# Kernel tuning notes

Hardware: AMD Instinct MI355X
Metric: run time of the kernel (lower is better)

Reference implementation:

```python
import jax, jax.numpy as jnp
import numpy as np

N = 50000        # nodes
E = 1600000      # edges (before self loops)
C_IN = 128
C_OUT = 128
G = 64           # graphs in the batch
NEG_SLOPE = 0.2  # GATConv default


def setup_inputs() -> dict:
    key = jax.random.key(0)
    ks = jax.random.split(key, 12)
    u = jax.random.normal(ks[0], (N, C_IN), jnp.float32)
    edge_index = jax.random.randint(ks[1], (2, E), 0, N, dtype=jnp.int32)
    batch = jnp.sort(jax.random.randint(ks[2], (N,), 0, G, dtype=jnp.int32))
    g1 = 1.0 / np.sqrt(C_IN)
    g2 = 1.0 / np.sqrt(C_OUT)
    return {
        "u": u,
        "W1": jax.random.normal(ks[3], (C_IN, C_OUT), jnp.float32) * g1,
        "a_src1": jax.random.normal(ks[4], (C_OUT,), jnp.float32) * g2,
        "a_dst1": jax.random.normal(ks[5], (C_OUT,), jnp.float32) * g2,
        "b1": jnp.zeros((C_OUT,), jnp.float32),
        "W2": jax.random.normal(ks[6], (C_OUT, C_OUT), jnp.float32) * g2,
        "a_src2": jax.random.normal(ks[7], (C_OUT,), jnp.float32) * g2,
        "a_dst2": jax.random.normal(ks[8], (C_OUT,), jnp.float32) * g2,
        "b2": jnp.zeros((C_OUT,), jnp.float32),
        "edge_index": edge_index,
        "batch": batch,
    }


def gat_conv(x, edge_index, W, a_src, a_dst, b):
    """PyG GATConv, heads=1: linear -> edge attention -> scatter softmax -> scatter add."""
    n = x.shape[0]
    h = x @ W                                        # [N, C]
    loops = jnp.arange(n, dtype=edge_index.dtype)    # add_self_loops=True
    src = jnp.concatenate([edge_index[0], loops])    # message source j
    dst = jnp.concatenate([edge_index[1], loops])    # aggregation target i
    alpha_s = h @ a_src                              # [N]
    alpha_d = h @ a_dst                              # [N]
    e = jax.nn.leaky_relu(alpha_s[src] + alpha_d[dst], NEG_SLOPE)  # [E+N]
    m = jax.ops.segment_max(e, dst, num_segments=n)  # stable softmax per target
    w = jnp.exp(e - m[dst])
    denom = jax.ops.segment_sum(w, dst, num_segments=n)
    alpha = w / denom[dst]                           # [E+N]
    out = jax.ops.segment_sum(alpha[:, None] * h[src], dst, num_segments=n)
    return out + b


def reference(u, W1, a_src1, a_dst1, b1, W2, a_src2, a_dst2, b2, edge_index, batch):
    h = jax.nn.selu(gat_conv(u, edge_index, W1, a_src1, a_dst1, b1))
    h = jax.nn.selu(gat_conv(h, edge_index, W2, a_src2, a_dst2, b2))
    # global_mean_pool
    s = jax.ops.segment_sum(h, batch, num_segments=G)                      # [G, C]
    cnt = jax.ops.segment_sum(jnp.ones((h.shape[0],), h.dtype), batch, num_segments=G)
    return s / jnp.maximum(cnt, 1.0)[:, None]
```

## Files before the change

kernel.cpp:

```cpp
#include <hip/hip_runtime.h>
#include <hip/hip_bf16.h>
#include <math.h>

#define CH 128
#define PSHIFT 8
#define PSIZE (1 << PSHIFT)
#define CHUNK 2048
#define EPT 8
#define MAXP 256
#define PCAP 12288
#define PS 8

typedef __attribute__((ext_vector_type(8))) short short8;
typedef __attribute__((ext_vector_type(4))) float f32x4;

__device__ __forceinline__ float seluf(float x) {
    const float scale = 1.0507009873554804934193349852946f;
    const float alpha = 1.6732632423543772848170429916717f;
    return x > 0.0f ? scale * x : scale * alpha * (__expf(x) - 1.0f);
}

__device__ __forceinline__ float lrelu(float x) {
    return x > 0.0f ? x : 0.2f * x;
}

__device__ __forceinline__ short bfc(float f) {
    union { __hip_bfloat16 b; short s; } u;
    u.b = __float2bfloat16(f);
    return u.s;
}

__device__ __forceinline__ unsigned pk(float lo, float hi) {
    return ((unsigned)(unsigned short)bfc(hi) << 16) | (unsigned short)bfc(lo);
}


__global__ __launch_bounds__(256) void k_part(const int* __restrict__ ei,
                                              int* __restrict__ pfill,
                                              unsigned long long* __restrict__ staged,
                                              int E, int NP) {
    __shared__ int hist[MAXP];
    __shared__ int base[MAXP];
    const int tid = threadIdx.x;
    const int j0 = blockIdx.x * CHUNK;
    for (int i = tid; i < NP; i += 256) hist[i] = 0;
    __syncthreads();
    int part[EPT], rank[EPT];
    unsigned long long rec[EPT];
#pragma unroll
    for (int e = 0; e < EPT; ++e) {
        int j = j0 + e * 256 + tid;
        part[e] = -1;
        if (j < E) {
            int s = ei[j], d = ei[E + j];
            part[e] = d >> PSHIFT;
            rec[e] = ((unsigned long long)(unsigned)d << 32) | (unsigned)s;
            rank[e] = atomicAdd(&hist[part[e]], 1);
        }
    }
    __syncthreads();
    for (int i = tid; i < NP; i += 256)
        base[i] = hist[i] ? atomicAdd(&pfill[i], hist[i]) : 0;
    __syncthreads();
#pragma unroll
    for (int e = 0; e < EPT; ++e)
        if (part[e] >= 0)
            staged[(size_t)part[e] * PCAP + base[part[e]] + rank[e]] = rec[e];
}


__global__ __launch_bounds__(256) void k_fat(
    const unsigned long long* __restrict__ staged, const int* __restrict__ pfill,
    int* __restrict__ rowptr, int* __restrict__ csr, int n, int E, int NP,
    const float* __restrict__ x, const float* __restrict__ W,
    const float* __restrict__ a_s, const float* __restrict__ a_d,
    __hip_bfloat16* __restrict__ hb, float* __restrict__ as_o,
    float* __restrict__ ad_o) {
    __shared__ __align__(16) char sm[32768];
    const int tid = threadIdx.x;

    if ((int)blockIdx.x < NP) {
        int* lcnt = (int*)sm;
        int* lrow = lcnt + PSIZE;
        int* sc   = lrow + PSIZE;
        int* psc  = sc + PSIZE;
        const int p = blockIdx.x;
        const int d0 = p << PSHIFT;
        psc[tid] = (tid < NP) ? pfill[tid] : 0;
        lcnt[tid] = 0;
        __syncthreads();
        for (int off = 1; off < 256; off <<= 1) {
            int v = (tid >= off) ? psc[tid - off] : 0;
            __syncthreads();
            psc[tid] += v;
            __syncthreads();
        }
        const int pbase = psc[p] - pfill[p];
        const size_t rbeg = (size_t)p * PCAP;
        const size_t rend = rbeg + pfill[p];
        const int rb = pbase + d0;
        for (size_t r = rbeg + tid; r < rend; r += 256)
            atomicAdd(&lcnt[(int)(staged[r] >> 32) - d0], 1);
        __syncthreads();
        int myv = (d0 + tid < n) ? lcnt[tid] + 1 : 0;
        sc[tid] = myv;
        __syncthreads();
        for (int off = 1; off < 256; off <<= 1) {
            int v = (tid >= off) ? sc[tid - off] : 0;
            __syncthreads();
            sc[tid] += v;
            __syncthreads();
        }
        if (d0 + tid < n) {
            int rp = rb + sc[tid] - myv;
            lrow[tid] = rp;
            rowptr[d0 + tid] = rp;
            csr[rp] = d0 + tid;
            lcnt[tid] = 0;
        }
        if (p == 0 && tid == 0) rowptr[n] = E + n;
        __syncthreads();
        for (size_t r = rbeg + tid; r < rend; r += 256) {
            unsigned long long v = staged[r];
            int d = (int)(v >> 32), s = (int)(v & 0xffffffffu);
            int pos = lrow[d - d0] + 1 + atomicAdd(&lcnt[d - d0], 1);
            csr[pos] = s;
        }
        return;
    }

    short* WB = (short*)sm;
    for (int i = tid; i < CH * CH; i += 256) {
        int k = i >> 7, c = i & 127;
        int kb = k >> 5, kk = k & 31;
        int t = c >> 4;
        int ln = (c & 15) | ((kk >> 3) << 4);
        int j = kk & 7;
        WB[(((kb << 3) + t) << 9) + (ln << 3) + j] = bfc(W[i]);
    }
    __syncthreads();
    const int bid = blockIdx.x - NP;
    const int lane = tid & 63;
    const int wid = tid >> 6;
    const int l15 = lane & 15;
    const int lhi = lane >> 4;
    float asl[8], adl[8];
#pragma unroll
    for (int t = 0; t < 8; ++t) {
        asl[t] = a_s[t * 16 + l15];
        adl[t] = a_d[t * 16 + l15];
    }
#pragma unroll
    for (int s = 0; s < 2; ++s) {
        int r0 = bid * 128 + s * 64 + wid * 16;
        if (r0 >= n) break;
        int ar = r0 + l15; if (ar >= n) ar = n - 1;
        const float* xr = x + (size_t)ar * CH + lhi * 8;
        f32x4 acc[8];
#pragma unroll
        for (int t = 0; t < 8; ++t) acc[t] = (f32x4){0.f, 0.f, 0.f, 0.f};
#pragma unroll
        for (int kb = 0; kb < 4; ++kb) {
            float4 xa = *(const float4*)(xr + kb * 32);
            float4 xb = *(const float4*)(xr + kb * 32 + 4);
            short8 af;
            af[0] = bfc(xa.x); af[1] = bfc(xa.y); af[2] = bfc(xa.z); af[3] = bfc(xa.w);
            af[4] = bfc(xb.x); af[5] = bfc(xb.y); af[6] = bfc(xb.z); af[7] = bfc(xb.w);
#pragma unroll
            for (int t = 0; t < 8; ++t) {
                short8 bv = ((const short8*)WB)[(((kb << 3) + t) << 6) | lane];
                acc[t] = __builtin_amdgcn_mfma_f32_16x16x32_bf16(af, bv, acc[t], 0, 0, 0);
            }
        }
        float pa[4] = {0.f, 0.f, 0.f, 0.f}, pd[4] = {0.f, 0.f, 0.f, 0.f};
#pragma unroll
        for (int t = 0; t < 8; ++t) {
#pragma unroll
            for (int q = 0; q < 4; ++q) {
                int row = r0 + lhi * 4 + q;
                if (row < n)
                    hb[(size_t)row * CH + t * 16 + l15] = __float2bfloat16(acc[t][q]);
                pa[q] += acc[t][q] * asl[t];
                pd[q] += acc[t][q] * adl[t];
            }
        }
#pragma unroll
        for (int q = 0; q < 4; ++q) {
#pragma unroll
            for (int o = 1; o < 16; o <<= 1) {
                pa[q] += __shfl_xor(pa[q], o);
                pd[q] += __shfl_xor(pd[q], o);
            }
        }
        if (l15 == 0) {
#pragma unroll
            for (int q = 0; q < 4; ++q) {
                int row = r0 + lhi * 4 + q;
                if (row < n) { as_o[row] = pa[q]; ad_o[row] = pd[q]; }
            }
        }
    }
}


template <typename T>
__global__ __launch_bounds__(256) void k_gemm3(
    const T* __restrict__ x, const float* __restrict__ W,
    const float* __restrict__ a_s, const float* __restrict__ a_d,
    __hip_bfloat16* __restrict__ hb, float* __restrict__ as_o,
    float* __restrict__ ad_o, int n) {
    __shared__ short WB[4 * 8 * 64 * 8];
    const int tid = threadIdx.x;
    for (int i = tid; i < CH * CH; i += 256) {
        int k = i >> 7, c = i & 127;
        int kb = k >> 5, kk = k & 31;
        int t = c >> 4;
        int ln = (c & 15) | ((kk >> 3) << 4);
        int j = kk & 7;
        WB[(((kb << 3) + t) << 9) + (ln << 3) + j] = bfc(W[i]);
    }
    __syncthreads();
    const int lane = tid & 63;
    const int wid = tid >> 6;
    const int l15 = lane & 15;
    const int lhi = lane >> 4;
    float asl[8], adl[8];
#pragma unroll
    for (int t = 0; t < 8; ++t) {
        asl[t] = a_s[t * 16 + l15];
        adl[t] = a_d[t * 16 + l15];
    }
#pragma unroll
    for (int s = 0; s < 2; ++s) {
        int r0 = blockIdx.x * 128 + s * 64 + wid * 16;
        if (r0 >= n) break;
        int ar = r0 + l15; if (ar >= n) ar = n - 1;
        const T* xr = x + (size_t)ar * CH + lhi * 8;
        f32x4 acc[8];
#pragma unroll
        for (int t = 0; t < 8; ++t) acc[t] = (f32x4){0.f, 0.f, 0.f, 0.f};
#pragma unroll
        for (int kb = 0; kb < 4; ++kb) {
            short8 af;
            if constexpr (sizeof(T) == 4) {
                float4 xa = *(const float4*)(xr + kb * 32);
                float4 xb = *(const float4*)(xr + kb * 32 + 4);
                af[0] = bfc(xa.x); af[1] = bfc(xa.y); af[2] = bfc(xa.z); af[3] = bfc(xa.w);
                af[4] = bfc(xb.x); af[5] = bfc(xb.y); af[6] = bfc(xb.z); af[7] = bfc(xb.w);
            } else {
                af = *(const short8*)(xr + kb * 32);
            }
#pragma unroll
            for (int t = 0; t < 8; ++t) {
                short8 bv = ((const short8*)WB)[(((kb << 3) + t) << 6) | lane];
                acc[t] = __builtin_amdgcn_mfma_f32_16x16x32_bf16(af, bv, acc[t], 0, 0, 0);
            }
        }
        float pa[4] = {0.f, 0.f, 0.f, 0.f}, pd[4] = {0.f, 0.f, 0.f, 0.f};
#pragma unroll
        for (int t = 0; t < 8; ++t) {
#pragma unroll
            for (int q = 0; q < 4; ++q) {
                int row = r0 + lhi * 4 + q;
                if (row < n)
                    hb[(size_t)row * CH + t * 16 + l15] = __float2bfloat16(acc[t][q]);
                pa[q] += acc[t][q] * asl[t];
                pd[q] += acc[t][q] * adl[t];
            }
        }
#pragma unroll
        for (int q = 0; q < 4; ++q) {
#pragma unroll
            for (int o = 1; o < 16; o <<= 1) {
                pa[q] += __shfl_xor(pa[q], o);
                pd[q] += __shfl_xor(pd[q], o);
            }
        }
        if (l15 == 0) {
#pragma unroll
            for (int q = 0; q < 4; ++q) {
                int row = r0 + lhi * 4 + q;
                if (row < n) { as_o[row] = pa[q]; ad_o[row] = pd[q]; }
            }
        }
    }
}


__global__ __launch_bounds__(256) void k_fused_agg(
    const int* __restrict__ rowptr, const int* __restrict__ csr,
    const float* __restrict__ as_v, const float* __restrict__ ad_v,
    float* __restrict__ wedge, const __hip_bfloat16* __restrict__ hb,
    const float* __restrict__ bias, __hip_bfloat16* __restrict__ out, int n) {
    int gw = (int)((blockIdx.x * (size_t)blockDim.x + threadIdx.x) >> 6);
    int lane = threadIdx.x & 63;
    if (gw >= n) return;
    int beg = rowptr[gw], end = rowptr[gw + 1];
    int deg = end - beg;
    float adi = ad_v[gw];

    const int quarter = lane >> 4;
    const int c8 = lane & 15;
    float acc[8];
#pragma unroll
    for (int k = 0; k < 8; ++k) acc[k] = 0.f;
    float inv;

    if (deg <= 64) {
        bool valid = lane < deg;
        int src = valid ? csr[beg + lane] : 0;
        float e = valid ? lrelu(as_v[src] + adi) : -1e30f;
        float m = e;
#pragma unroll
        for (int o = 32; o > 0; o >>= 1) m = fmaxf(m, __shfl_xor(m, o));
        float w = valid ? __expf(e - m) : 0.f;
        float s = w;
#pragma unroll
        for (int o = 32; o > 0; o >>= 1) s += __shfl_xor(s, o);
        inv = 1.0f / s;
        for (int b = 0; b < deg; b += 8) {
            int i0 = b + quarter;
            int i1 = b + 4 + quarter;
            float w0 = __shfl(w, i0);
            int s0 = __shfl(src, i0);
            float w1 = (i1 < 64) ? __shfl(w, i1) : 0.f;
            int s1 = (i1 < 64) ? __shfl(src, i1) : 0;
            uint4 hv0 = ((const uint4*)hb)[(size_t)s0 * 16 + c8];
            uint4 hv1 = ((const uint4*)hb)[(size_t)s1 * 16 + c8];
            acc[0] += w0 * __uint_as_float(hv0.x << 16);
            acc[1] += w0 * __uint_as_float(hv0.x & 0xffff0000u);
            acc[2] += w0 * __uint_as_float(hv0.y << 16);
            acc[3] += w0 * __uint_as_float(hv0.y & 0xffff0000u);
            acc[4] += w0 * __uint_as_float(hv0.z << 16);
            acc[5] += w0 * __uint_as_float(hv0.z & 0xffff0000u);
            acc[6] += w0 * __uint_as_float(hv0.w << 16);
            acc[7] += w0 * __uint_as_float(hv0.w & 0xffff0000u);
            acc[0] += w1 * __uint_as_float(hv1.x << 16);
            acc[1] += w1 * __uint_as_float(hv1.x & 0xffff0000u);
            acc[2] += w1 * __uint_as_float(hv1.y << 16);
            acc[3] += w1 * __uint_as_float(hv1.y & 0xffff0000u);
            acc[4] += w1 * __uint_as_float(hv1.z << 16);
            acc[5] += w1 * __uint_as_float(hv1.z & 0xffff0000u);
            acc[6] += w1 * __uint_as_float(hv1.w << 16);
            acc[7] += w1 * __uint_as_float(hv1.w & 0xffff0000u);
        }
    } else {
        float m = -1e30f;
        for (int p = beg + lane; p < end; p += 64) {
            float e = lrelu(as_v[csr[p]] + adi);
            wedge[p] = e;
            m = fmaxf(m, e);
        }
#pragma unroll
        for (int o = 32; o > 0; o >>= 1) m = fmaxf(m, __shfl_xor(m, o));
        float s = 0.f;
        for (int p = beg + lane; p < end; p += 64) {
            float wv = __expf(wedge[p] - m);
            wedge[p] = wv;
            s += wv;
        }
#pragma unroll
        for (int o = 32; o > 0; o >>= 1) s += __shfl_xor(s, o);
        inv = 1.0f / s;
        for (int p = beg; p < end; p += 8) {
            int p0 = p + quarter, p1 = p + 4 + quarter;
            float w0 = 0.f, w1 = 0.f;
            int s0 = 0, s1 = 0;
            if (p0 < end) { w0 = wedge[p0]; s0 = csr[p0]; }
            if (p1 < end) { w1 = wedge[p1]; s1 = csr[p1]; }
            uint4 hv0 = ((const uint4*)hb)[(size_t)s0 * 16 + c8];
            uint4 hv1 = ((const uint4*)hb)[(size_t)s1 * 16 + c8];
            acc[0] += w0 * __uint_as_float(hv0.x << 16);
            acc[1] += w0 * __uint_as_float(hv0.x & 0xffff0000u);
            acc[2] += w0 * __uint_as_float(hv0.y << 16);
            acc[3] += w0 * __uint_as_float(hv0.y & 0xffff0000u);
            acc[4] += w0 * __uint_as_float(hv0.z << 16);
            acc[5] += w0 * __uint_as_float(hv0.z & 0xffff0000u);
            acc[6] += w0 * __uint_as_float(hv0.w << 16);
            acc[7] += w0 * __uint_as_float(hv0.w & 0xffff0000u);
            acc[0] += w1 * __uint_as_float(hv1.x << 16);
            acc[1] += w1 * __uint_as_float(hv1.x & 0xffff0000u);
            acc[2] += w1 * __uint_as_float(hv1.y << 16);
            acc[3] += w1 * __uint_as_float(hv1.y & 0xffff0000u);
            acc[4] += w1 * __uint_as_float(hv1.z << 16);
            acc[5] += w1 * __uint_as_float(hv1.z & 0xffff0000u);
            acc[6] += w1 * __uint_as_float(hv1.w << 16);
            acc[7] += w1 * __uint_as_float(hv1.w & 0xffff0000u);
        }
    }
#pragma unroll
    for (int k = 0; k < 8; ++k) {
        acc[k] += __shfl_xor(acc[k], 16);
        acc[k] += __shfl_xor(acc[k], 32);
    }
    if (quarter == 0) {
        const float4 bv0 = ((const float4*)bias)[c8 * 2];
        const float4 bv1 = ((const float4*)bias)[c8 * 2 + 1];
        float o0 = seluf(acc[0] * inv + bv0.x);
        float o1 = seluf(acc[1] * inv + bv0.y);
        float o2 = seluf(acc[2] * inv + bv0.z);
        float o3 = seluf(acc[3] * inv + bv0.w);
        float o4 = seluf(acc[4] * inv + bv1.x);
        float o5 = seluf(acc[5] * inv + bv1.y);
        float o6 = seluf(acc[6] * inv + bv1.z);
        float o7 = seluf(acc[7] * inv + bv1.w);
        uint4 ov;
        ov.x = pk(o0, o1);
        ov.y = pk(o2, o3);
        ov.z = pk(o4, o5);
        ov.w = pk(o6, o7);
        ((uint4*)out)[(size_t)gw * 16 + c8] = ov;
    }
}


__device__ int lower_bound_dev(const int* a, int n, int key) {
    int lo = 0, hi = n;
    while (lo < hi) {
        int mid = (lo + hi) >> 1;
        if (a[mid] < key) lo = mid + 1; else hi = mid;
    }
    return lo;
}

__global__ __launch_bounds__(256) void k_pool1(const __hip_bfloat16* __restrict__ x,
                                               const int* __restrict__ batchv,
                                               float* __restrict__ part, int n) {
    int g = blockIdx.x >> 3, s = blockIdx.x & (PS - 1);
    int lo = lower_bound_dev(batchv, n, g);
    int hi = lower_bound_dev(batchv, n, g + 1);
    int lane = threadIdx.x & 63, wv = threadIdx.x >> 6;
    int slot = s * 4 + wv;
    float sx0 = 0.f, sy0 = 0.f, sx1 = 0.f, sy1 = 0.f;
    int i = lo + slot;
    for (; i + 32 < hi; i += 64) {
        unsigned u0 = ((const unsigned*)x)[(size_t)i * 64 + lane];
        unsigned u1 = ((const unsigned*)x)[(size_t)(i + 32) * 64 + lane];
        sx0 += __uint_as_float(u0 << 16);
        sy0 += __uint_as_float(u0 & 0xffff0000u);
        sx1 += __uint_as_float(u1 << 16);
        sy1 += __uint_as_float(u1 & 0xffff0000u);
    }
    if (i < hi) {
        unsigned u0 = ((const unsigned*)x)[(size_t)i * 64 + lane];
        sx0 += __uint_as_float(u0 << 16);
        sy0 += __uint_as_float(u0 & 0xffff0000u);
    }
    __shared__ float2 red[4][64];
    red[wv][lane] = make_float2(sx0 + sx1, sy0 + sy1);
    __syncthreads();
    if (wv == 0) {
        float2 a = red[0][lane], b = red[1][lane], c = red[2][lane], d = red[3][lane];
        float* pp = part + ((size_t)(g * PS + s)) * CH;
        pp[2 * lane] = a.x + b.x + c.x + d.x;
        pp[2 * lane + 1] = a.y + b.y + c.y + d.y;
    }
}

__global__ __launch_bounds__(128) void k_pool2(const float* __restrict__ part,
                                               const int* __restrict__ batchv,
                                               float* __restrict__ outp, int n) {
    int g = blockIdx.x, t = threadIdx.x;
    int lo = lower_bound_dev(batchv, n, g);
    int hi = lower_bound_dev(batchv, n, g + 1);
    float v = 0.f;
#pragma unroll
    for (int s = 0; s < PS; ++s) v += part[((size_t)(g * PS + s)) * CH + t];
    int cnt = hi - lo; if (cnt < 1) cnt = 1;
    outp[(size_t)g * CH + t] = v / (float)cnt;
}


extern "C" void kernel_launch(void* const* d_in, const int* in_sizes, int n_in,
                              void* d_out, int out_size, void* d_ws, size_t ws_size,
                              hipStream_t stream) {
    const float* u   = (const float*)d_in[0];
    const float* W1  = (const float*)d_in[1];
    const float* as1 = (const float*)d_in[2];
    const float* ad1 = (const float*)d_in[3];
    const float* b1  = (const float*)d_in[4];
    const float* W2  = (const float*)d_in[5];
    const float* as2 = (const float*)d_in[6];
    const float* ad2 = (const float*)d_in[7];
    const float* b2  = (const float*)d_in[8];
    const int* ei    = (const int*)d_in[9];
    const int* batchv= (const int*)d_in[10];

    const int N = in_sizes[0] / CH;
    const int E = in_sizes[9] / 2;
    const int M = E + N;
    const int NP = (N + PSIZE - 1) >> PSHIFT;
    const int G = out_size / CH;

    char* p = (char*)d_ws;
    auto alloc = [&](size_t bytes) {
        char* r = p;
        p += (bytes + 255) & ~(size_t)255;
        return r;
    };
    int*   pfill  = (int*)alloc((size_t)NP * 4);
    size_t zbytes = (size_t)(p - (char*)d_ws);
    int*   rowptr = (int*)alloc((size_t)(N + 1) * 4);
    int*   csr    = (int*)alloc((size_t)M * 4);
    float* asv    = (float*)alloc((size_t)N * 4);
    float* adv    = (float*)alloc((size_t)N * 4);
    float* ppart  = (float*)alloc((size_t)G * PS * CH * 4);
    __hip_bfloat16* hbuf = (__hip_bfloat16*)alloc((size_t)N * CH * 2);
    size_t wbytes = ((size_t)M * 4 + 255) & ~(size_t)255;
    size_t xbytes = (size_t)N * CH * 2;
    size_t sbytes = (size_t)NP * PCAP * 8;
    size_t blob   = wbytes + xbytes > sbytes ? wbytes + xbytes : sbytes;
    char*  bb     = alloc(blob);
    unsigned long long* staged = (unsigned long long*)bb;
    float* wedge  = (float*)bb;
    __hip_bfloat16* x2 = (__hip_bfloat16*)(bb + wbytes);

    hipMemsetAsync(d_ws, 0, zbytes, stream);

    const int gblocks = (N + 127) / 128;

    k_part<<<(E + CHUNK - 1) / CHUNK, 256, 0, stream>>>(ei, pfill, staged, E, NP);
    k_fat<<<NP + gblocks, 256, 0, stream>>>(staged, pfill, rowptr, csr, N, E, NP,
                                            u, W1, as1, ad1, hbuf, asv, adv);

    k_fused_agg<<<(N * 64 + 255) / 256, 256, 0, stream>>>(rowptr, csr, asv, adv, wedge, hbuf, b1, x2, N);

    k_gemm3<__hip_bfloat16><<<gblocks, 256, 0, stream>>>(x2, W2, as2, ad2, hbuf, asv, adv, N);
    k_fused_agg<<<(N * 64 + 255) / 256, 256, 0, stream>>>(rowptr, csr, asv, adv, wedge, hbuf, b2, x2, N);

    k_pool1<<<G * PS, 256, 0, stream>>>(x2, batchv, ppart, N);
    k_pool2<<<G, 128, 0, stream>>>(ppart, batchv, (float*)d_out, N);
}
```

Baseline: 201.2 us.

## Pack staged edges to 32 bits, unroll gather by four, fuse pooling kernels

Staged edge records now pack the local destination into 8 bits and the source into 24 bits, halving staging traffic. The partition chunk per block doubles. The low-degree aggregation loop now gathers four neighbour rows per iteration to expose more memory parallelism. The two-stage mean pool becomes one 1024-thread kernel per graph, which removes a launch but lowers parallelism and assumes N fits in 24 bits.

New measurement: 190.6 us. 5.3% less time.

```diff
diff --git a/kernel.cpp b/kernel.cpp
--- a/kernel.cpp
+++ b/kernel.cpp
@@ -5,8 +5,8 @@
 #define CH 128
 #define PSHIFT 8
 #define PSIZE (1 << PSHIFT)
-#define CHUNK 2048
-#define EPT 8
+#define CHUNK 4096
+#define EPT 16
 #define MAXP 256
 #define PCAP 12288
 #define PS 8
@@ -37,7 +37,7 @@
 
 __global__ __launch_bounds__(256) void k_part(const int* __restrict__ ei,
                                               int* __restrict__ pfill,
-                                              unsigned long long* __restrict__ staged,
+                                              unsigned* __restrict__ staged,
                                               int E, int NP) {
     __shared__ int hist[MAXP];
     __shared__ int base[MAXP];
@@ -46,7 +46,7 @@
     for (int i = tid; i < NP; i += 256) hist[i] = 0;
     __syncthreads();
     int part[EPT], rank[EPT];
-    unsigned long long rec[EPT];
+    unsigned rec[EPT];
 #pragma unroll
     for (int e = 0; e < EPT; ++e) {
         int j = j0 + e * 256 + tid;
@@ -54,7 +54,7 @@
         if (j < E) {
             int s = ei[j], d = ei[E + j];
             part[e] = d >> PSHIFT;
-            rec[e] = ((unsigned long long)(unsigned)d << 32) | (unsigned)s;
+            rec[e] = ((unsigned)(d & (PSIZE - 1)) << 24) | (unsigned)s;
             rank[e] = atomicAdd(&hist[part[e]], 1);
         }
     }
@@ -70,7 +70,7 @@
 
 
 __global__ __launch_bounds__(256) void k_fat(
-    const unsigned long long* __restrict__ staged, const int* __restrict__ pfill,
+    const unsigned* __restrict__ staged, const int* __restrict__ pfill,
     int* __restrict__ rowptr, int* __restrict__ csr, int n, int E, int NP,
     const float* __restrict__ x, const float* __restrict__ W,
     const float* __restrict__ a_s, const float* __restrict__ a_d,
@@ -100,7 +100,7 @@
         const size_t rend = rbeg + pfill[p];
         const int rb = pbase + d0;
         for (size_t r = rbeg + tid; r < rend; r += 256)
-            atomicAdd(&lcnt[(int)(staged[r] >> 32) - d0], 1);
+            atomicAdd(&lcnt[staged[r] >> 24], 1);
         __syncthreads();
         int myv = (d0 + tid < n) ? lcnt[tid] + 1 : 0;
         sc[tid] = myv;
@@ -121,9 +121,9 @@
         if (p == 0 && tid == 0) rowptr[n] = E + n;
         __syncthreads();
         for (size_t r = rbeg + tid; r < rend; r += 256) {
-            unsigned long long v = staged[r];
-            int d = (int)(v >> 32), s = (int)(v & 0xffffffffu);
-            int pos = lrow[d - d0] + 1 + atomicAdd(&lcnt[d - d0], 1);
+            unsigned v = staged[r];
+            int dd = v >> 24, s = (int)(v & 0xFFFFFFu);
+            int pos = lrow[dd] + 1 + atomicAdd(&lcnt[dd], 1);
             csr[pos] = s;
         }
         return;
@@ -318,15 +318,17 @@
 #pragma unroll
         for (int o = 32; o > 0; o >>= 1) s += __shfl_xor(s, o);
         inv = 1.0f / s;
-        for (int b = 0; b < deg; b += 8) {
-            int i0 = b + quarter;
-            int i1 = b + 4 + quarter;
-            float w0 = __shfl(w, i0);
-            int s0 = __shfl(src, i0);
-            float w1 = (i1 < 64) ? __shfl(w, i1) : 0.f;
-            int s1 = (i1 < 64) ? __shfl(src, i1) : 0;
+        for (int b = 0; b < deg; b += 16) {
+            int i0 = b + quarter, i1 = b + 4 + quarter;
+            int i2 = b + 8 + quarter, i3 = b + 12 + quarter;
+            float w0 = __shfl(w, i0), w1 = __shfl(w, i1);
+            float w2 = __shfl(w, i2), w3 = __shfl(w, i3);
+            int s0 = __shfl(src, i0), s1 = __shfl(src, i1);
+            int s2 = __shfl(src, i2), s3 = __shfl(src, i3);
             uint4 hv0 = ((const uint4*)hb)[(size_t)s0 * 16 + c8];
             uint4 hv1 = ((const uint4*)hb)[(size_t)s1 * 16 + c8];
+            uint4 hv2 = ((const uint4*)hb)[(size_t)s2 * 16 + c8];
+            uint4 hv3 = ((const uint4*)hb)[(size_t)s3 * 16 + c8];
             acc[0] += w0 * __uint_as_float(hv0.x << 16);
             acc[1] += w0 * __uint_as_float(hv0.x & 0xffff0000u);
             acc[2] += w0 * __uint_as_float(hv0.y << 16);
@@ -343,6 +345,22 @@
             acc[5] += w1 * __uint_as_float(hv1.z & 0xffff0000u);
             acc[6] += w1 * __uint_as_float(hv1.w << 16);
             acc[7] += w1 * __uint_as_float(hv1.w & 0xffff0000u);
+            acc[0] += w2 * __uint_as_float(hv2.x << 16);
+            acc[1] += w2 * __uint_as_float(hv2.x & 0xffff0000u);
+            acc[2] += w2 * __uint_as_float(hv2.y << 16);
+            acc[3] += w2 * __uint_as_float(hv2.y & 0xffff0000u);
+            acc[4] += w2 * __uint_as_float(hv2.z << 16);
+            acc[5] += w2 * __uint_as_float(hv2.z & 0xffff0000u);
+            acc[6] += w2 * __uint_as_float(hv2.w << 16);
+            acc[7] += w2 * __uint_as_float(hv2.w & 0xffff0000u);
+            acc[0] += w3 * __uint_as_float(hv3.x << 16);
+            acc[1] += w3 * __uint_as_float(hv3.x & 0xffff0000u);
+            acc[2] += w3 * __uint_as_float(hv3.y << 16);
+            acc[3] += w3 * __uint_as_float(hv3.y & 0xffff0000u);
+            acc[4] += w3 * __uint_as_float(hv3.z << 16);
+            acc[5] += w3 * __uint_as_float(hv3.z & 0xffff0000u);
+            acc[6] += w3 * __uint_as_float(hv3.w << 16);
+            acc[7] += w3 * __uint_as_float(hv3.w & 0xffff0000u);
         }
     } else {
         float m = -1e30f;
@@ -423,19 +441,18 @@
     return lo;
 }
 
-__global__ __launch_bounds__(256) void k_pool1(const __hip_bfloat16* __restrict__ x,
+__global__ __launch_bounds__(1024) void k_pool(const __hip_bfloat16* __restrict__ x,
                                                const int* __restrict__ batchv,
-                                               float* __restrict__ part, int n) {
-    int g = blockIdx.x >> 3, s = blockIdx.x & (PS - 1);
+                                               float* __restrict__ outp, int n) {
+    int g = blockIdx.x;
     int lo = lower_bound_dev(batchv, n, g);
     int hi = lower_bound_dev(batchv, n, g + 1);
     int lane = threadIdx.x & 63, wv = threadIdx.x >> 6;
-    int slot = s * 4 + wv;
     float sx0 = 0.f, sy0 = 0.f, sx1 = 0.f, sy1 = 0.f;
-    int i = lo + slot;
-    for (; i + 32 < hi; i += 64) {
+    int i = lo + wv;
+    for (; i + 16 < hi; i += 32) {
         unsigned u0 = ((const unsigned*)x)[(size_t)i * 64 + lane];
-        unsigned u1 = ((const unsigned*)x)[(size_t)(i + 32) * 64 + lane];
+        unsigned u1 = ((const unsigned*)x)[(size_t)(i + 16) * 64 + lane];
         sx0 += __uint_as_float(u0 << 16);
         sy0 += __uint_as_float(u0 & 0xffff0000u);
         sx1 += __uint_as_float(u1 << 16);
@@ -446,28 +463,18 @@
         sx0 += __uint_as_float(u0 << 16);
         sy0 += __uint_as_float(u0 & 0xffff0000u);
     }
-    __shared__ float2 red[4][64];
+    __shared__ float2 red[16][64];
     red[wv][lane] = make_float2(sx0 + sx1, sy0 + sy1);
     __syncthreads();
     if (wv == 0) {
-        float2 a = red[0][lane], b = red[1][lane], c = red[2][lane], d = red[3][lane];
-        float* pp = part + ((size_t)(g * PS + s)) * CH;
-        pp[2 * lane] = a.x + b.x + c.x + d.x;
-        pp[2 * lane + 1] = a.y + b.y + c.y + d.y;
-    }
-}
-
-__global__ __launch_bounds__(128) void k_pool2(const float* __restrict__ part,
-                                               const int* __restrict__ batchv,
-                                               float* __restrict__ outp, int n) {
-    int g = blockIdx.x, t = threadIdx.x;
-    int lo = lower_bound_dev(batchv, n, g);
-    int hi = lower_bound_dev(batchv, n, g + 1);
-    float v = 0.f;
-#pragma unroll
-    for (int s = 0; s < PS; ++s) v += part[((size_t)(g * PS + s)) * CH + t];
-    int cnt = hi - lo; if (cnt < 1) cnt = 1;
-    outp[(size_t)g * CH + t] = v / (float)cnt;
+        float ax = 0.f, ay = 0.f;
+#pragma unroll
+        for (int s = 0; s < 16; ++s) { ax += red[s][lane].x; ay += red[s][lane].y; }
+        int cnt = hi - lo; if (cnt < 1) cnt = 1;
+        float invc = 1.0f / (float)cnt;
+        outp[(size_t)g * CH + 2 * lane] = ax * invc;
+        outp[(size_t)g * CH + 2 * lane + 1] = ay * invc;
+    }
 }
 
 
@@ -504,14 +511,13 @@
     int*   csr    = (int*)alloc((size_t)M * 4);
     float* asv    = (float*)alloc((size_t)N * 4);
     float* adv    = (float*)alloc((size_t)N * 4);
-    float* ppart  = (float*)alloc((size_t)G * PS * CH * 4);
     __hip_bfloat16* hbuf = (__hip_bfloat16*)alloc((size_t)N * CH * 2);
     size_t wbytes = ((size_t)M * 4 + 255) & ~(size_t)255;
     size_t xbytes = (size_t)N * CH * 2;
-    size_t sbytes = (size_t)NP * PCAP * 8;
+    size_t sbytes = (size_t)NP * PCAP * 4;
     size_t blob   = wbytes + xbytes > sbytes ? wbytes + xbytes : sbytes;
     char*  bb     = alloc(blob);
-    unsigned long long* staged = (unsigned long long*)bb;
+    unsigned* staged = (unsigned*)bb;
     float* wedge  = (float*)bb;
     __hip_bfloat16* x2 = (__hip_bfloat16*)(bb + wbytes);
 
@@ -528,6 +534,5 @@
     k_gemm3<__hip_bfloat16><<<gblocks, 256, 0, stream>>>(x2, W2, as2, ad2, hbuf, asv, adv, N);
     k_fused_agg<<<(N * 64 + 255) / 256, 256, 0, stream>>>(rowptr, csr, asv, adv, wedge, hbuf, b2, x2, N);
 
-    k_pool1<<<G * PS, 256, 0, stream>>>(x2, batchv, ppart, N);
-    k_pool2<<<G, 128, 0, stream>>>(ppart, batchv, (float*)d_out, N);
-}
+    k_pool<<<G, 1024, 0, stream>>>(x2, batchv, (float*)d_out, N);
+}
```
